# Optimization experiments

Measured on AMD Instinct MI355X. Metric: run time of the kernel, lower is better.

The kernel has to match this reference:

```python
import jax, jax.numpy as jnp
import numpy as np

B, T, D, HS = 8, 2048, 1024, 64

def setup_inputs() -> dict:
    key = jax.random.key(0)
    ks = jax.random.split(key, 7)
    s = 1.0 / np.sqrt(D)
    return {
        "x": jax.random.normal(ks[0], (B, T, D), dtype=jnp.float32),
        "wq_w": jax.random.normal(ks[1], (HS, D), dtype=jnp.float32) * s,
        "wq_b": jax.random.normal(ks[2], (HS,), dtype=jnp.float32) * 0.01,
        "wk_w": jax.random.normal(ks[3], (HS, D), dtype=jnp.float32) * s,
        "wk_b": jax.random.normal(ks[4], (HS,), dtype=jnp.float32) * 0.01,
        "wv_w": jax.random.normal(ks[5], (HS, D), dtype=jnp.float32) * s,
        "wv_b": jax.random.normal(ks[6], (HS,), dtype=jnp.float32) * 0.01,
    }

def reference(x, wq_w, wq_b, wk_w, wk_b, wv_w, wv_b):
    Tq = x.shape[1]
    q = jnp.einsum('btd,hd->bth', x, wq_w) + wq_b  # [B,T,HS]
    k = jnp.einsum('btd,hd->bth', x, wk_w) + wk_b
    v = jnp.einsum('btd,hd->bth', x, wv_w) + wv_b
    scores = jnp.einsum('bth,bsh->bts', q, k) / jnp.sqrt(jnp.float32(HS))  # [B,T,T]
    causal = jnp.tril(jnp.ones((Tq, Tq), dtype=bool))
    scores = jnp.where(causal, scores, -jnp.inf)
    weight = jax.nn.softmax(scores, axis=-1)
    # dropout p=0.0 -> identity
    out = jnp.einsum('bts,bsh->bth', weight, v)  # [B,T,HS]
    return out
```

## Files before the change

kernel.cpp:

```cpp
#include <hip/hip_runtime.h>

#define DD 1024
#define HSZ 64
#define TT 2048
#define NB 8
#define MM (NB*TT)

typedef unsigned short U16;
typedef U16 u16x4 __attribute__((ext_vector_type(4)));
typedef U16 u16x8 __attribute__((ext_vector_type(8)));
typedef float f32x4 __attribute__((ext_vector_type(4)));

__device__ inline U16 f2b(float f) {
    unsigned u = __builtin_bit_cast(unsigned, f);
    u += 0x7FFFu + ((u >> 16) & 1u);
    return (U16)(u >> 16);
}

__device__ inline f32x4 mfma16(u16x8 a, u16x8 b, f32x4 c) {
    return __builtin_amdgcn_mfma_f32_16x16x32_bf16(a, b, c, 0, 0, 0);
}

__device__ inline void gld16(const void* g, void* l) {
    __builtin_amdgcn_global_load_lds(
        (const __attribute__((address_space(1))) void*)g,
        (__attribute__((address_space(3))) void*)l, 16, 0, 0);
}

__global__ __launch_bounds__(256) void wconv_kernel(
    const float* __restrict__ wq, const float* __restrict__ wk,
    const float* __restrict__ wv, U16* __restrict__ wb)
{
    int t = blockIdx.x * 256 + threadIdx.x;
    int n = t >> 8;
    int k0 = (t & 255) * 4;
    const float* src = n < 64 ? wq + (size_t)n * DD
                     : (n < 128 ? wk + (size_t)(n - 64) * DD
                                : wv + (size_t)(n - 128) * DD);
    float4 v = *(const float4*)(src + k0);
    int chunk = k0 >> 7, kc = k0 & 127;
    int byte = (n * 256 + kc * 2) ^ ((n & 7) << 4);
    u16x4 h = { f2b(v.x), f2b(v.y), f2b(v.z), f2b(v.w) };
    *(u16x4*)((char*)wb + (size_t)chunk * 49152 + byte) = h;
}

__global__ __launch_bounds__(512) void qkv_kernel(
    const float* __restrict__ x, const U16* __restrict__ wb,
    const float* __restrict__ wqb, const float* __restrict__ wkb, const float* __restrict__ wvb,
    U16* __restrict__ qb, U16* __restrict__ kb, U16* __restrict__ vt)
{
    __shared__ __attribute__((aligned(16))) U16 Bs[2][24576];
    __shared__ __attribute__((aligned(16))) U16 As[2][8192];

    const int tid = threadIdx.x, lane = tid & 63, w = tid >> 6;
    const int wm = w >> 1, wn = w & 1, g = lane >> 4, c = lane & 15;
    const int m0 = blockIdx.x * 64;

    const int arow = tid >> 3, aseg = tid & 7;
    const float* axp = x + (size_t)(m0 + arow) * DD + aseg * 16;
    const int abyte0 = (arow * 256 + aseg * 32) ^ ((arow & 7) << 4);
    const int abyte1 = (arow * 256 + aseg * 32 + 16) ^ ((arow & 7) << 4);

    f32x4 acc[6] = {};
    float4 ar0, ar1, ar2, ar3;

    {
        const float* p = axp;
        ar0 = *(const float4*)(p); ar1 = *(const float4*)(p + 4);
        ar2 = *(const float4*)(p + 8); ar3 = *(const float4*)(p + 12);
        const char* src = (const char*)wb + tid * 16;
        char* dst = (char*)&Bs[0][0] + tid * 16;
        #pragma unroll
        for (int it = 0; it < 6; ++it) gld16(src + it * 8192, dst + it * 8192);
        u16x8 h0 = { f2b(ar0.x), f2b(ar0.y), f2b(ar0.z), f2b(ar0.w),
                     f2b(ar1.x), f2b(ar1.y), f2b(ar1.z), f2b(ar1.w) };
        u16x8 h1 = { f2b(ar2.x), f2b(ar2.y), f2b(ar2.z), f2b(ar2.w),
                     f2b(ar3.x), f2b(ar3.y), f2b(ar3.z), f2b(ar3.w) };
        *(u16x8*)((char*)&As[0][0] + abyte0) = h0;
        *(u16x8*)((char*)&As[0][0] + abyte1) = h1;
    }
    __syncthreads();

    for (int ch = 0; ch < 8; ++ch) {
        const int cur = ch & 1, nxt = cur ^ 1;
        if (ch < 7) {
            const float* p = axp + (ch + 1) * 128;
            ar0 = *(const float4*)(p); ar1 = *(const float4*)(p + 4);
            ar2 = *(const float4*)(p + 8); ar3 = *(const float4*)(p + 12);
            const char* src = (const char*)wb + (size_t)(ch + 1) * 49152 + tid * 16;
            char* dst = (char*)&Bs[nxt][0] + tid * 16;
            #pragma unroll
            for (int it = 0; it < 6; ++it) gld16(src + it * 8192, dst + it * 8192);
        }
        #pragma unroll
        for (int ks = 0; ks < 4; ++ks) {
            const int rl = wm * 16 + c;
            u16x8 af = *(const u16x8*)((const char*)&As[cur][0] +
                        ((rl * 256 + ks * 64 + g * 16) ^ ((c & 7) << 4)));
            #pragma unroll
            for (int nf = 0; nf < 6; ++nf) {
                const int n = wn * 96 + nf * 16 + c;
                u16x8 bf = *(const u16x8*)((const char*)&Bs[cur][0] +
                            ((n * 256 + ks * 64 + g * 16) ^ ((n & 7) << 4)));
                acc[nf] = mfma16(af, bf, acc[nf]);
            }
        }
        if (ch < 7) {
            u16x8 h0 = { f2b(ar0.x), f2b(ar0.y), f2b(ar0.z), f2b(ar0.w),
                         f2b(ar1.x), f2b(ar1.y), f2b(ar1.z), f2b(ar1.w) };
            u16x8 h1 = { f2b(ar2.x), f2b(ar2.y), f2b(ar2.z), f2b(ar2.w),
                         f2b(ar3.x), f2b(ar3.y), f2b(ar3.z), f2b(ar3.w) };
            *(u16x8*)((char*)&As[nxt][0] + abyte0) = h0;
            *(u16x8*)((char*)&As[nxt][0] + abyte1) = h1;
        }
        __syncthreads();
    }

    #pragma unroll
    for (int nf = 0; nf < 6; ++nf) {
        const int col = wn * 96 + nf * 16 + c;
        const int head = col >> 6, h = col & 63;
        const float bv = head == 0 ? wqb[h] : (head == 1 ? wkb[h] : wvb[h]);
        #pragma unroll
        for (int r = 0; r < 4; ++r) {
            const int row = m0 + wm * 16 + g * 4 + r;
            const float val = acc[nf][r] + bv;
            if (head == 0)      qb[(size_t)row * HSZ + h] = f2b(val * 0.125f);
            else if (head == 1) kb[(size_t)row * HSZ + h] = f2b(val);
            else {
                const int b = row >> 11, tok = row & 2047;
                vt[(size_t)b * (HSZ * TT) + (size_t)h * TT + tok] = f2b(val);
            }
        }
    }
}

__global__ __launch_bounds__(256) void attn_kernel(
    const U16* __restrict__ qb, const U16* __restrict__ kb, const U16* __restrict__ vt,
    float* __restrict__ out)
{
    __shared__ __attribute__((aligned(16))) U16 Ps[4][1024];

    const int tid = threadIdx.x, lane = tid & 63, w = tid >> 6;
    const int g = lane >> 4, c = lane & 15;
    const int jid = blockIdx.x * 4 + w;
    const int batch = jid & 7, j = jid >> 3;
    const int q0 = j * 16;
    const size_t base = (size_t)batch * TT;
    char* psw = (char*)&Ps[w][0];

    u16x8 aq[2];
    {
        const U16* qp = qb + (base + q0 + c) * HSZ;
        aq[0] = *(const u16x8*)(qp + g * 8);
        aq[1] = *(const u16x8*)(qp + 32 + g * 8);
    }

    f32x4 acc[4] = {};
    float mrow[4] = {-1e30f, -1e30f, -1e30f, -1e30f};
    float lrow[4] = {};
    const int nt = (j >> 2) + 1;
    const U16* vbase = vt + (size_t)batch * HSZ * TT;

    for (int t = 0; t < nt; ++t) {
        const size_t kvb = base + (size_t)t * 64;
        f32x4 s[4] = {};
        #pragma unroll
        for (int ks = 0; ks < 2; ++ks)
            #pragma unroll
            for (int nf = 0; nf < 4; ++nf) {
                u16x8 kf = *(const u16x8*)(kb + (kvb + nf * 16 + c) * HSZ + ks * 32 + g * 8);
                s[nf] = mfma16(aq[ks], kf, s[nf]);
            }
        u16x8 vf[2][4];
        #pragma unroll
        for (int ks = 0; ks < 2; ++ks)
            #pragma unroll
            for (int nf = 0; nf < 4; ++nf)
                vf[ks][nf] = *(const u16x8*)(vbase + (size_t)(nf * 16 + c) * TT + t * 64 + ks * 32 + g * 8);

        if (t == nt - 1) {
            #pragma unroll
            for (int nf = 0; nf < 4; ++nf)
                #pragma unroll
                for (int r = 0; r < 4; ++r)
                    if (t * 64 + nf * 16 + c > q0 + g * 4 + r) s[nf][r] = -1e30f;
        }

        float pv[4][4];
        #pragma unroll
        for (int r = 0; r < 4; ++r) {
            float pm = fmaxf(fmaxf(s[0][r], s[1][r]), fmaxf(s[2][r], s[3][r]));
            pm = fmaxf(pm, __shfl_xor(pm, 1));
            pm = fmaxf(pm, __shfl_xor(pm, 2));
            pm = fmaxf(pm, __shfl_xor(pm, 4));
            pm = fmaxf(pm, __shfl_xor(pm, 8));
            const float mn = fmaxf(mrow[r], pm);
            const float sc = __expf(mrow[r] - mn);
            mrow[r] = mn;
            float rs = 0.f;
            #pragma unroll
            for (int nf = 0; nf < 4; ++nf) { pv[nf][r] = __expf(s[nf][r] - mn); rs += pv[nf][r]; }
            rs += __shfl_xor(rs, 1); rs += __shfl_xor(rs, 2);
            rs += __shfl_xor(rs, 4); rs += __shfl_xor(rs, 8);
            lrow[r] = lrow[r] * sc + rs;
            acc[0][r] *= sc; acc[1][r] *= sc; acc[2][r] *= sc; acc[3][r] *= sc;
        }

        #pragma unroll
        for (int nf = 0; nf < 4; ++nf)
            #pragma unroll
            for (int r = 0; r < 4; ++r) {
                const int row = g * 4 + r, col = nf * 16 + c;
                *(U16*)(psw + ((row * 128 + col * 2) ^ ((row & 7) << 4))) = f2b(pv[nf][r]);
            }
        u16x8 pa[2];
        #pragma unroll
        for (int ks = 0; ks < 2; ++ks)
            pa[ks] = *(const u16x8*)(psw + ((c * 128 + ks * 64 + g * 16) ^ ((c & 7) << 4)));

        #pragma unroll
        for (int ks = 0; ks < 2; ++ks)
            #pragma unroll
            for (int nf = 0; nf < 4; ++nf)
                acc[nf] = mfma16(pa[ks], vf[ks][nf], acc[nf]);
    }

    #pragma unroll
    for (int nf = 0; nf < 4; ++nf)
        #pragma unroll
        for (int r = 0; r < 4; ++r)
            out[(base + q0 + g * 4 + r) * HSZ + nf * 16 + c] = acc[nf][r] / lrow[r];
}

extern "C" void kernel_launch(void* const* d_in, const int* in_sizes, int n_in,
                              void* d_out, int out_size, void* d_ws, size_t ws_size,
                              hipStream_t stream) {
    const float* x   = (const float*)d_in[0];
    const float* wq  = (const float*)d_in[1];
    const float* wqb = (const float*)d_in[2];
    const float* wk  = (const float*)d_in[3];
    const float* wkb = (const float*)d_in[4];
    const float* wv  = (const float*)d_in[5];
    const float* wvb = (const float*)d_in[6];
    float* out = (float*)d_out;

    U16* wb = (U16*)d_ws;
    U16* qb = wb + 196608;
    U16* kb = qb + (size_t)MM * HSZ;
    U16* vt = kb + (size_t)MM * HSZ;

    wconv_kernel<<<192, 256, 0, stream>>>(wq, wk, wv, wb);
    qkv_kernel<<<256, 512, 0, stream>>>(x, wb, wqb, wkb, wvb, qb, kb, vt);
    attn_kernel<<<256, 256, 0, stream>>>(qb, kb, vt, out);
}
```

Measured before the change: 178.2 us.

## Split attention KV range across waves with combine kernel; shrink QKV tiles

The attention kernel now splits each query tile's causal KV range into chunks of four 64-key tiles (flash-decoding style). Each wave writes unnormalized partial outputs plus running max and sum to a workspace, and a new combine kernel merges them with log-sum-exp rescaling. This spreads the long causal rows over more blocks to fix load imbalance and low occupancy, at the cost of extra workspace traffic and one more launch. The QKV projection also moves to 32-row tiles with 64-wide K chunks and 256 threads, doubling the block count for better CU coverage.

```diff
diff --git a/kernel.cpp b/kernel.cpp
--- a/kernel.cpp
+++ b/kernel.cpp
@@ -5,6 +5,7 @@
 #define TT 2048
 #define NB 8
 #define MM (NB*TT)
+#define PART_STRIDE 1056
 
 typedef unsigned short U16;
 typedef U16 u16x4 __attribute__((ext_vector_type(4)));
@@ -38,80 +39,71 @@
                      : (n < 128 ? wk + (size_t)(n - 64) * DD
                                 : wv + (size_t)(n - 128) * DD);
     float4 v = *(const float4*)(src + k0);
-    int chunk = k0 >> 7, kc = k0 & 127;
-    int byte = (n * 256 + kc * 2) ^ ((n & 7) << 4);
+    int chunk = k0 >> 6, kc = k0 & 63;
+    int byte = (n * 128 + kc * 2) ^ ((n & 7) << 4);
     u16x4 h = { f2b(v.x), f2b(v.y), f2b(v.z), f2b(v.w) };
-    *(u16x4*)((char*)wb + (size_t)chunk * 49152 + byte) = h;
-}
-
-__global__ __launch_bounds__(512) void qkv_kernel(
+    *(u16x4*)((char*)wb + (size_t)chunk * 24576 + byte) = h;
+}
+
+__global__ __launch_bounds__(256) void qkv_kernel(
     const float* __restrict__ x, const U16* __restrict__ wb,
     const float* __restrict__ wqb, const float* __restrict__ wkb, const float* __restrict__ wvb,
     U16* __restrict__ qb, U16* __restrict__ kb, U16* __restrict__ vt)
 {
-    __shared__ __attribute__((aligned(16))) U16 Bs[2][24576];
-    __shared__ __attribute__((aligned(16))) U16 As[2][8192];
+    __shared__ __attribute__((aligned(16))) U16 Bs[2][12288];
+    __shared__ __attribute__((aligned(16))) U16 As[2][2048];
 
     const int tid = threadIdx.x, lane = tid & 63, w = tid >> 6;
     const int wm = w >> 1, wn = w & 1, g = lane >> 4, c = lane & 15;
-    const int m0 = blockIdx.x * 64;
+    const int m0 = blockIdx.x * 32;
 
     const int arow = tid >> 3, aseg = tid & 7;
-    const float* axp = x + (size_t)(m0 + arow) * DD + aseg * 16;
-    const int abyte0 = (arow * 256 + aseg * 32) ^ ((arow & 7) << 4);
-    const int abyte1 = (arow * 256 + aseg * 32 + 16) ^ ((arow & 7) << 4);
+    const float* axp = x + (size_t)(m0 + arow) * DD + aseg * 8;
+    const int abyte = (arow * 128 + aseg * 16) ^ ((arow & 7) << 4);
 
     f32x4 acc[6] = {};
-    float4 ar0, ar1, ar2, ar3;
+    float4 ar0, ar1;
 
     {
-        const float* p = axp;
-        ar0 = *(const float4*)(p); ar1 = *(const float4*)(p + 4);
-        ar2 = *(const float4*)(p + 8); ar3 = *(const float4*)(p + 12);
+        ar0 = *(const float4*)(axp);
+        ar1 = *(const float4*)(axp + 4);
         const char* src = (const char*)wb + tid * 16;
         char* dst = (char*)&Bs[0][0] + tid * 16;
         #pragma unroll
-        for (int it = 0; it < 6; ++it) gld16(src + it * 8192, dst + it * 8192);
-        u16x8 h0 = { f2b(ar0.x), f2b(ar0.y), f2b(ar0.z), f2b(ar0.w),
-                     f2b(ar1.x), f2b(ar1.y), f2b(ar1.z), f2b(ar1.w) };
-        u16x8 h1 = { f2b(ar2.x), f2b(ar2.y), f2b(ar2.z), f2b(ar2.w),
-                     f2b(ar3.x), f2b(ar3.y), f2b(ar3.z), f2b(ar3.w) };
-        *(u16x8*)((char*)&As[0][0] + abyte0) = h0;
-        *(u16x8*)((char*)&As[0][0] + abyte1) = h1;
+        for (int it = 0; it < 6; ++it) gld16(src + it * 4096, dst + it * 4096);
+        u16x8 h = { f2b(ar0.x), f2b(ar0.y), f2b(ar0.z), f2b(ar0.w),
+                    f2b(ar1.x), f2b(ar1.y), f2b(ar1.z), f2b(ar1.w) };
+        *(u16x8*)((char*)&As[0][0] + abyte) = h;
     }
     __syncthreads();
 
-    for (int ch = 0; ch < 8; ++ch) {
+    for (int ch = 0; ch < 16; ++ch) {
         const int cur = ch & 1, nxt = cur ^ 1;
-        if (ch < 7) {
-            const float* p = axp + (ch + 1) * 128;
+        if (ch < 15) {
+            const float* p = axp + (ch + 1) * 64;
             ar0 = *(const float4*)(p); ar1 = *(const float4*)(p + 4);
-            ar2 = *(const float4*)(p + 8); ar3 = *(const float4*)(p + 12);
-            const char* src = (const char*)wb + (size_t)(ch + 1) * 49152 + tid * 16;
+            const char* src = (const char*)wb + (size_t)(ch + 1) * 24576 + tid * 16;
             char* dst = (char*)&Bs[nxt][0] + tid * 16;
             #pragma unroll
-            for (int it = 0; it < 6; ++it) gld16(src + it * 8192, dst + it * 8192);
-        }
-        #pragma unroll
-        for (int ks = 0; ks < 4; ++ks) {
+            for (int it = 0; it < 6; ++it) gld16(src + it * 4096, dst + it * 4096);
+        }
+        #pragma unroll
+        for (int ks = 0; ks < 2; ++ks) {
             const int rl = wm * 16 + c;
             u16x8 af = *(const u16x8*)((const char*)&As[cur][0] +
-                        ((rl * 256 + ks * 64 + g * 16) ^ ((c & 7) << 4)));
+                        ((rl * 128 + ks * 64 + g * 16) ^ ((rl & 7) << 4)));
             #pragma unroll
             for (int nf = 0; nf < 6; ++nf) {
                 const int n = wn * 96 + nf * 16 + c;
                 u16x8 bf = *(const u16x8*)((const char*)&Bs[cur][0] +
-                            ((n * 256 + ks * 64 + g * 16) ^ ((n & 7) << 4)));
+                            ((n * 128 + ks * 64 + g * 16) ^ ((n & 7) << 4)));
                 acc[nf] = mfma16(af, bf, acc[nf]);
             }
         }
-        if (ch < 7) {
-            u16x8 h0 = { f2b(ar0.x), f2b(ar0.y), f2b(ar0.z), f2b(ar0.w),
-                         f2b(ar1.x), f2b(ar1.y), f2b(ar1.z), f2b(ar1.w) };
-            u16x8 h1 = { f2b(ar2.x), f2b(ar2.y), f2b(ar2.z), f2b(ar2.w),
-                         f2b(ar3.x), f2b(ar3.y), f2b(ar3.z), f2b(ar3.w) };
-            *(u16x8*)((char*)&As[nxt][0] + abyte0) = h0;
-            *(u16x8*)((char*)&As[nxt][0] + abyte1) = h1;
+        if (ch < 15) {
+            u16x8 h = { f2b(ar0.x), f2b(ar0.y), f2b(ar0.z), f2b(ar0.w),
+                        f2b(ar1.x), f2b(ar1.y), f2b(ar1.z), f2b(ar1.w) };
+            *(u16x8*)((char*)&As[nxt][0] + abyte) = h;
         }
         __syncthreads();
     }
@@ -137,16 +129,24 @@
 
 __global__ __launch_bounds__(256) void attn_kernel(
     const U16* __restrict__ qb, const U16* __restrict__ kb, const U16* __restrict__ vt,
-    float* __restrict__ out)
+    float* __restrict__ part)
 {
     __shared__ __attribute__((aligned(16))) U16 Ps[4][1024];
 
     const int tid = threadIdx.x, lane = tid & 63, w = tid >> 6;
     const int g = lane >> 4, c = lane & 15;
     const int jid = blockIdx.x * 4 + w;
-    const int batch = jid & 7, j = jid >> 3;
+    const int chunk = jid & 7;
+    const int j = (jid >> 3) & 127;
+    const int batch = jid >> 10;
+    const int a = j >> 4;
+    if (chunk > a) return;
+
     const int q0 = j * 16;
     const size_t base = (size_t)batch * TT;
+    const int nt = (j >> 2) + 1;
+    const int t0 = chunk * 4;
+    const int t_end = (chunk == a) ? nt : t0 + 4;
     char* psw = (char*)&Ps[w][0];
 
     u16x8 aq[2];
@@ -159,10 +159,9 @@
     f32x4 acc[4] = {};
     float mrow[4] = {-1e30f, -1e30f, -1e30f, -1e30f};
     float lrow[4] = {};
-    const int nt = (j >> 2) + 1;
     const U16* vbase = vt + (size_t)batch * HSZ * TT;
 
-    for (int t = 0; t < nt; ++t) {
+    for (int t = t0; t < t_end; ++t) {
         const size_t kvb = base + (size_t)t * 64;
         f32x4 s[4] = {};
         #pragma unroll
@@ -226,11 +225,43 @@
                 acc[nf] = mfma16(pa[ks], vf[ks][nf], acc[nf]);
     }
 
+    const int slot = batch * 576 + (a + 1) * (8 * a + (j & 15)) + chunk;
+    float* sp = part + (size_t)slot * PART_STRIDE;
     #pragma unroll
     for (int nf = 0; nf < 4; ++nf)
         #pragma unroll
         for (int r = 0; r < 4; ++r)
-            out[(base + q0 + g * 4 + r) * HSZ + nf * 16 + c] = acc[nf][r] / lrow[r];
+            sp[(g * 4 + r) * 64 + nf * 16 + c] = acc[nf][r];
+    if (c == 0) {
+        #pragma unroll
+        for (int r = 0; r < 4; ++r) {
+            sp[1024 + g * 4 + r] = mrow[r];
+            sp[1040 + g * 4 + r] = lrow[r];
+        }
+    }
+}
+
+__global__ __launch_bounds__(256) void combine_kernel(
+    const float* __restrict__ part, float* __restrict__ out)
+{
+    const int j = blockIdx.x, batch = blockIdx.y;
+    const int a = j >> 4, nc = a + 1;
+    const int slot0 = batch * 576 + (a + 1) * (8 * a + (j & 15));
+    const int t = threadIdx.x, row = t >> 4, sg = t & 15;
+    const float* sp = part + (size_t)slot0 * PART_STRIDE;
+
+    float M = -1e30f;
+    for (int i = 0; i < nc; ++i) M = fmaxf(M, sp[i * PART_STRIDE + 1024 + row]);
+    float ox = 0.f, oy = 0.f, oz = 0.f, ow = 0.f, L = 0.f;
+    for (int i = 0; i < nc; ++i) {
+        const float wgt = __expf(sp[i * PART_STRIDE + 1024 + row] - M);
+        L += wgt * sp[i * PART_STRIDE + 1040 + row];
+        const float4 ov = *(const float4*)&sp[i * PART_STRIDE + row * 64 + sg * 4];
+        ox += wgt * ov.x; oy += wgt * ov.y; oz += wgt * ov.z; ow += wgt * ov.w;
+    }
+    const float inv = 1.f / L;
+    float4 res = { ox * inv, oy * inv, oz * inv, ow * inv };
+    *(float4*)&out[((size_t)batch * TT + j * 16 + row) * HSZ + sg * 4] = res;
 }
 
 extern "C" void kernel_launch(void* const* d_in, const int* in_sizes, int n_in,
@@ -249,8 +280,10 @@
     U16* qb = wb + 196608;
     U16* kb = qb + (size_t)MM * HSZ;
     U16* vt = kb + (size_t)MM * HSZ;
+    float* part = (float*)(vt + (size_t)MM * HSZ);
 
     wconv_kernel<<<192, 256, 0, stream>>>(wq, wk, wv, wb);
-    qkv_kernel<<<256, 512, 0, stream>>>(x, wb, wqb, wkb, wvb, qb, kb, vt);
-    attn_kernel<<<256, 256, 0, stream>>>(qb, kb, vt, out);
-}
+    qkv_kernel<<<512, 256, 0, stream>>>(x, wb, wqb, wkb, wvb, qb, kb, vt);
+    attn_kernel<<<2048, 256, 0, stream>>>(qb, kb, vt, part);
+    combine_kernel<<<dim3(128, NB), 256, 0, stream>>>(part, out);
+}
```

After: 182.4 us. 2.4% more time.
